# Performance work log

Hardware: AMD Instinct MI355X
Metric: run time of the kernel (lower is better)

Reference implementation:

```python
import jax, jax.numpy as jnp
import numpy as np

EMBED_DIM = 1024
HEAD_SIZE = 64
BATCH = 8
SEQ = 2048


def setup_inputs() -> dict:
    key = jax.random.key(0)
    k1, k2, k3, k4 = jax.random.split(key, 4)
    x = jax.random.normal(k1, (BATCH, SEQ, EMBED_DIM), dtype=jnp.float32)
    # Dense(use_bias=False) kernels: [in, out]
    scale = 1.0 / np.sqrt(EMBED_DIM)
    Wq = jax.random.normal(k2, (EMBED_DIM, HEAD_SIZE), dtype=jnp.float32) * scale
    Wk = jax.random.normal(k3, (EMBED_DIM, HEAD_SIZE), dtype=jnp.float32) * scale
    Wv = jax.random.normal(k4, (EMBED_DIM, HEAD_SIZE), dtype=jnp.float32) * scale
    return {"x": x, "Wq": Wq, "Wk": Wk, "Wv": Wv}


def reference(x, Wq, Wk, Wv):
    B, S, E = x.shape
    q = jnp.einsum("bse,eh->bsh", x, Wq)
    k = jnp.einsum("bse,eh->bsh", x, Wk)
    v = jnp.einsum("bse,eh->bsh", x, Wv)
    # scores scaled by embedding_dim**-0.5 (as in the original code)
    w = jnp.einsum("bqh,bkh->bqk", q, k) * (E ** -0.5)
    causal = jnp.tril(jnp.ones((S, S), dtype=bool))  # True on/below diag
    w = jnp.where(causal, w, -jnp.inf)
    w = jax.nn.softmax(w, axis=-1)
    # dropout is identity at inference
    return jnp.einsum("bqk,bkh->bqh", w, v)
```

## Files before the change

### kernel.cpp

```cpp
#include <hip/hip_runtime.h>
#include <hip/hip_bf16.h>


#define BATCH 8
#define SEQ   2048
#define EMB   1024
#define HD    64
#define ROWS  (BATCH*SEQ)
#define NTOT  192
#define BK    64
#define NKT   (EMB / BK)

typedef __attribute__((ext_vector_type(8))) short short8;
typedef __attribute__((ext_vector_type(4))) float floatx4;

static __device__ __forceinline__ short f2bf(float f) {
  union { __hip_bfloat16 h; short s; } u;
  u.h = __float2bfloat16(f);
  return u.s;
}

static __device__ __forceinline__ short8 pack8(float4 u, float4 v) {
  short8 r;
  r[0] = f2bf(u.x); r[1] = f2bf(u.y); r[2] = f2bf(u.z); r[3] = f2bf(u.w);
  r[4] = f2bf(v.x); r[5] = f2bf(v.y); r[6] = f2bf(v.z); r[7] = f2bf(v.w);
  return r;
}

static __device__ __forceinline__ void gload_lds16(const void* g, void* l) {
  __builtin_amdgcn_global_load_lds(
      (const __attribute__((address_space(1))) unsigned int*)g,
      (__attribute__((address_space(3))) unsigned int*)l, 16, 0, 0);
}

__global__ __launch_bounds__(256) void wt_kernel(
    const float* __restrict__ Wq, const float* __restrict__ Wk,
    const float* __restrict__ Wv, short* __restrict__ Wts) {
  const int id = blockIdx.x * 256 + threadIdx.x;
  const int kt = id / 1536;
  const int rem = id - kt * 1536;
  const int np = rem >> 3;
  const int s = rem & 7;
  const float* __restrict__ W = (np < 64) ? Wq : ((np < 128) ? Wk : Wv);
  const int n = np & 63;
  const int k0 = kt * BK + (s ^ (np & 7)) * 8;
  short8 o;
#pragma unroll
  for (int u = 0; u < 8; ++u) o[u] = f2bf(W[(size_t)(k0 + u) * HD + n]);
  *(short8*)(Wts + (size_t)id * 8) = o;
}

__global__ __launch_bounds__(256, 2) void proj_kernel(
    const float* __restrict__ x, const short* __restrict__ Wts,
    short* __restrict__ qb, short* __restrict__ kb_, short* __restrict__ vtb) {
  __shared__ __align__(16) float As[32 * 64];
  __shared__ __align__(16) short Bs[192 * 64];

  const int t = threadIdx.x, lane = t & 63, w = t >> 6;
  const int lo = lane & 15, quad = lane >> 4;
  const int e = lo & 7;
  const int m0 = blockIdx.x * 32;

  const int cc0 = w * 2, cc1 = cc0 + 1;
  const int ar0 = cc0 * 4 + (lane >> 4);
  const int ar1 = cc1 * 4 + (lane >> 4);
  const int aj = lane & 15;
  const float* agp0 = x + (size_t)(m0 + ar0) * EMB + ((aj ^ (ar0 & 7)) * 4);
  const float* agp1 = x + (size_t)(m0 + ar1) * EMB + ((aj ^ (ar1 & 7)) * 4);
  float* alp0 = As + cc0 * 256;
  float* alp1 = As + cc1 * 256;

  const short* bgp = Wts + (size_t)(w * 6) * 512 + lane * 8;
  short* blp = Bs + (w * 6) * 512;

  floatx4 acc[2][3];
#pragma unroll
  for (int mf = 0; mf < 2; ++mf)
#pragma unroll
    for (int j = 0; j < 3; ++j) acc[mf][j] = (floatx4){0.f, 0.f, 0.f, 0.f};

  for (int kt = 0; kt < NKT; ++kt) {
    __syncthreads();
    gload_lds16(agp0 + kt * BK, alp0);
    gload_lds16(agp1 + kt * BK, alp1);
    const short* bg = bgp + (size_t)kt * 12288;
#pragma unroll
    for (int i = 0; i < 6; ++i)
      gload_lds16(bg + i * 512, blp + i * 512);
    __syncthreads();

    short8 af[2][2];
#pragma unroll
    for (int mf = 0; mf < 2; ++mf) {
      const float* Ar = As + (mf * 16 + lo) * 64;
#pragma unroll
      for (int ks = 0; ks < 2; ++ks) {
        const float4 f0 = *(const float4*)(Ar + (((8 * ks + 2 * quad) ^ e) << 2));
        const float4 f1 = *(const float4*)(Ar + (((8 * ks + 2 * quad + 1) ^ e) << 2));
        af[mf][ks] = pack8(f0, f1);
      }
    }
    short8 bf[3][2];
#pragma unroll
    for (int j = 0; j < 3; ++j) {
      const short* Br = Bs + ((w * 3 + j) * 16 + lo) * 64;
#pragma unroll
      for (int ks = 0; ks < 2; ++ks)
        bf[j][ks] = *(const short8*)(Br + (((4 * ks + quad) ^ e) << 3));
    }
#pragma unroll
    for (int ks = 0; ks < 2; ++ks)
#pragma unroll
      for (int j = 0; j < 3; ++j) {
        acc[0][j] = __builtin_amdgcn_mfma_f32_16x16x32_bf16(af[0][ks], bf[j][ks], acc[0][j], 0, 0, 0);
        acc[1][j] = __builtin_amdgcn_mfma_f32_16x16x32_bf16(af[1][ks], bf[j][ks], acc[1][j], 0, 0, 0);
      }
  }

  const int bb = m0 >> 11;
  const int sbase = (m0 & (SEQ - 1)) + quad * 4;
#pragma unroll
  for (int mf = 0; mf < 2; ++mf) {
    const int rowb = m0 + mf * 16 + quad * 4;
#pragma unroll
    for (int j = 0; j < 3; ++j) {
      const int nt = w * 3 + j;
      const floatx4 v = acc[mf][j];
      if (nt < 4) {
#pragma unroll
        for (int r = 0; r < 4; ++r)
          qb[(size_t)(rowb + r) * HD + nt * 16 + lo] = f2bf(v[r] * 0.03125f);
      } else if (nt < 8) {
#pragma unroll
        for (int r = 0; r < 4; ++r)
          kb_[(size_t)(rowb + r) * HD + (nt - 4) * 16 + lo] = f2bf(v[r]);
      } else {
        const int col = (nt - 8) * 16 + lo;
        short4 sv = make_short4(f2bf(v[0]), f2bf(v[1]), f2bf(v[2]), f2bf(v[3]));
        *(short4*)(vtb + ((size_t)bb * HD + col) * SEQ + sbase + mf * 16) = sv;
      }
    }
  }
}

#define KSTR 72
#define PSTR 40

__global__ __launch_bounds__(256, 2) void attn_kernel(
    const short* __restrict__ qb, const short* __restrict__ kb,
    const short* __restrict__ vtb, float* __restrict__ out) {
  __shared__ __align__(16) short Ks[2][64 * KSTR];
  __shared__ __align__(16) short Vs[2][64 * KSTR];
  __shared__ __align__(16) short Ps[4][16 * PSTR];
  __shared__ __align__(16) floatx4 Red[2][5][64];

  const int b = blockIdx.y;
  const int bx = blockIdx.x;
  const int qx = (bx & 1) ? (63 - (bx >> 1)) : (bx >> 1);
  const int q0 = qx * 32;
  const int t = threadIdx.x, lane = t & 63, w = t >> 6;
  const int wr = w >> 1, wk = w & 1;
  const int lo = lane & 15, quad = lane >> 4;

  const short* qp = qb + ((size_t)b * SEQ + q0 + wr * 16 + lo) * HD + quad * 8;
  const short8 qf0 = *(const short8*)(qp);
  const short8 qf1 = *(const short8*)(qp + 32);

  const int r0 = t >> 3, c0 = (t & 7) * 8;
  const int r1 = r0 + 32;
  const short* __restrict__ kgb = kb + (size_t)b * SEQ * HD;
  const short* __restrict__ vgb = vtb + (size_t)b * HD * SEQ;

  floatx4 acc[4];
  float lsum[4] = {0.f, 0.f, 0.f, 0.f};
#pragma unroll
  for (int nt = 0; nt < 4; ++nt) acc[nt] = (floatx4){0.f, 0.f, 0.f, 0.f};

  {
    short8 k0v = *(const short8*)(kgb + (size_t)r0 * HD + c0);
    short8 k1v = *(const short8*)(kgb + (size_t)r1 * HD + c0);
    short8 v0v = *(const short8*)(vgb + (size_t)r0 * SEQ + c0);
    short8 v1v = *(const short8*)(vgb + (size_t)r1 * SEQ + c0);
    *(short8*)(&Ks[0][r0 * KSTR + c0]) = k0v;
    *(short8*)(&Ks[0][r1 * KSTR + c0]) = k1v;
    *(short8*)(&Vs[0][r0 * KSTR + c0]) = v0v;
    *(short8*)(&Vs[0][r1 * KSTR + c0]) = v1v;
  }

  const int niter = q0 / 64 + 1;
  for (int it = 0; it < niter; ++it) {
    const int j0 = it * 64;
    const int buf = it & 1;
    __syncthreads();

    short8 kfr[2][2], vfr[4];
#pragma unroll
    for (int n2 = 0; n2 < 2; ++n2) {
      const short* kr = &Ks[buf][(wk * 32 + n2 * 16 + lo) * KSTR + quad * 8];
      kfr[n2][0] = *(const short8*)(kr);
      kfr[n2][1] = *(const short8*)(kr + 32);
    }
#pragma unroll
    for (int nt = 0; nt < 4; ++nt)
      vfr[nt] = *(const short8*)(&Vs[buf][(nt * 16 + lo) * KSTR + wk * 32 + quad * 8]);

    short8 nk0, nk1, nv0, nv1;
    const bool more = (it + 1 < niter);
    if (more) {
      const int jn = j0 + 64;
      nk0 = *(const short8*)(kgb + (size_t)(jn + r0) * HD + c0);
      nk1 = *(const short8*)(kgb + (size_t)(jn + r1) * HD + c0);
      nv0 = *(const short8*)(vgb + (size_t)r0 * SEQ + jn + c0);
      nv1 = *(const short8*)(vgb + (size_t)r1 * SEQ + jn + c0);
    }

    floatx4 s0 = (floatx4){0.f, 0.f, 0.f, 0.f};
    floatx4 s1 = (floatx4){0.f, 0.f, 0.f, 0.f};
    s0 = __builtin_amdgcn_mfma_f32_16x16x32_bf16(qf0, kfr[0][0], s0, 0, 0, 0);
    s0 = __builtin_amdgcn_mfma_f32_16x16x32_bf16(qf1, kfr[0][1], s0, 0, 0, 0);
    s1 = __builtin_amdgcn_mfma_f32_16x16x32_bf16(qf0, kfr[1][0], s1, 0, 0, 0);
    s1 = __builtin_amdgcn_mfma_f32_16x16x32_bf16(qf1, kfr[1][1], s1, 0, 0, 0);

    const bool diag = (j0 + 64 > q0);
    const int rowb = q0 + wr * 16 + quad * 4;
    short* Pw = Ps[w];
#pragma unroll
    for (int r = 0; r < 4; ++r) {
      float e0 = __expf(s0[r]);
      float e1 = __expf(s1[r]);
      if (diag) {
        const int key0 = j0 + wk * 32 + lo;
        e0 = (key0 <= rowb + r) ? e0 : 0.f;
        e1 = (key0 + 16 <= rowb + r) ? e1 : 0.f;
      }
      lsum[r] += e0 + e1;
      Pw[(quad * 4 + r) * PSTR + lo] = f2bf(e0);
      Pw[(quad * 4 + r) * PSTR + 16 + lo] = f2bf(e1);
    }
    const short8 pf = *(const short8*)(&Pw[lo * PSTR + quad * 8]);
#pragma unroll
    for (int nt = 0; nt < 4; ++nt)
      acc[nt] = __builtin_amdgcn_mfma_f32_16x16x32_bf16(pf, vfr[nt], acc[nt], 0, 0, 0);

    if (more) {
      const int nb = buf ^ 1;
      *(short8*)(&Ks[nb][r0 * KSTR + c0]) = nk0;
      *(short8*)(&Ks[nb][r1 * KSTR + c0]) = nk1;
      *(short8*)(&Vs[nb][r0 * KSTR + c0]) = nv0;
      *(short8*)(&Vs[nb][r1 * KSTR + c0]) = nv1;
    }
  }

#pragma unroll
  for (int d = 1; d < 16; d <<= 1) {
#pragma unroll
    for (int r = 0; r < 4; ++r) lsum[r] += __shfl_xor(lsum[r], d);
  }

  if (wk == 1) {
#pragma unroll
    for (int nt = 0; nt < 4; ++nt) Red[wr][nt][lane] = acc[nt];
    Red[wr][4][lane] = (floatx4){lsum[0], lsum[1], lsum[2], lsum[3]};
  }
  __syncthreads();
  if (wk == 0) {
    const floatx4 lp = Red[wr][4][lane];
    const int rowb = q0 + wr * 16 + quad * 4;
#pragma unroll
    for (int nt = 0; nt < 4; ++nt) {
      const floatx4 o = acc[nt] + Red[wr][nt][lane];
#pragma unroll
      for (int r = 0; r < 4; ++r)
        out[((size_t)b * SEQ + rowb + r) * HD + nt * 16 + lo] =
            o[r] / (lsum[r] + lp[r]);
    }
  }
}

extern "C" void kernel_launch(void* const* d_in, const int* in_sizes, int n_in,
                              void* d_out, int out_size, void* d_ws, size_t ws_size,
                              hipStream_t stream) {
  const float* x  = (const float*)d_in[0];
  const float* Wq = (const float*)d_in[1];
  const float* Wk = (const float*)d_in[2];
  const float* Wv = (const float*)d_in[3];
  float* out = (float*)d_out;
  short* ws = (short*)d_ws;
  short* qbp = ws;
  short* kbp = ws + (size_t)ROWS * HD;
  short* vtp = ws + (size_t)2 * ROWS * HD;
  short* Wts = ws + (size_t)3 * ROWS * HD;

  wt_kernel<<<dim3(96), 256, 0, stream>>>(Wq, Wk, Wv, Wts);
  proj_kernel<<<dim3(ROWS / 32), 256, 0, stream>>>(x, Wts, qbp, kbp, vtp);
  attn_kernel<<<dim3(SEQ / 32, BATCH), 256, 0, stream>>>(qbp, kbp, vtp, out);
}
```

Measured before the change: 145.0 us.

## Shrink attention query tile to 16 rows and load K/V directly into swizzled LDS

The attention kernel now gives each block 16 query rows and two waves instead of 32 rows and four waves, which doubles the number of blocks. K and V tiles are copied with direct global-to-LDS loads into an XOR-swizzled layout with no padding, replacing register staging with a double buffer. The aim is to raise occupancy and cut register and VGPR traffic for tile loads. In exchange, every K/V tile is fetched by twice as many blocks, and the load is no longer prefetched, so each iteration adds a second barrier and exposes load latency.

```diff
diff --git a/kernel.cpp b/kernel.cpp
--- a/kernel.cpp
+++ b/kernel.cpp
@@ -143,75 +143,65 @@
   }
 }
 
-#define KSTR 72
+#define QT 16
 #define PSTR 40
 
-__global__ __launch_bounds__(256, 2) void attn_kernel(
+__global__ __launch_bounds__(128, 4) void attn_kernel(
     const short* __restrict__ qb, const short* __restrict__ kb,
     const short* __restrict__ vtb, float* __restrict__ out) {
-  __shared__ __align__(16) short Ks[2][64 * KSTR];
-  __shared__ __align__(16) short Vs[2][64 * KSTR];
-  __shared__ __align__(16) short Ps[4][16 * PSTR];
-  __shared__ __align__(16) floatx4 Red[2][5][64];
+  __shared__ __align__(16) short Ks[64 * 64];
+  __shared__ __align__(16) short Vs[64 * 64];
+  __shared__ __align__(16) short Ps[2][16 * PSTR];
+  __shared__ __align__(16) floatx4 Red[5][64];
 
   const int b = blockIdx.y;
   const int bx = blockIdx.x;
-  const int qx = (bx & 1) ? (63 - (bx >> 1)) : (bx >> 1);
-  const int q0 = qx * 32;
+  const int qx = (bx & 1) ? (127 - (bx >> 1)) : (bx >> 1);
+  const int q0 = qx * QT;
   const int t = threadIdx.x, lane = t & 63, w = t >> 6;
-  const int wr = w >> 1, wk = w & 1;
-  const int lo = lane & 15, quad = lane >> 4;
-
-  const short* qp = qb + ((size_t)b * SEQ + q0 + wr * 16 + lo) * HD + quad * 8;
+  const int lo = lane & 15, quad = lane >> 4, e = lo & 7;
+
+  const short* qp = qb + ((size_t)b * SEQ + q0 + lo) * HD + quad * 8;
   const short8 qf0 = *(const short8*)(qp);
   const short8 qf1 = *(const short8*)(qp + 32);
 
-  const int r0 = t >> 3, c0 = (t & 7) * 8;
-  const int r1 = r0 + 32;
-  const short* __restrict__ kgb = kb + (size_t)b * SEQ * HD;
-  const short* __restrict__ vgb = vtb + (size_t)b * HD * SEQ;
+  const int sr = lane >> 3;
+  const int jg = (lane & 7) ^ (sr & 7);
+  const short* kaddr = kb + (size_t)b * SEQ * HD + sr * HD + jg * 8;
+  const short* vaddr = vtb + (size_t)b * HD * SEQ + (size_t)sr * SEQ + jg * 8;
 
   floatx4 acc[4];
   float lsum[4] = {0.f, 0.f, 0.f, 0.f};
 #pragma unroll
   for (int nt = 0; nt < 4; ++nt) acc[nt] = (floatx4){0.f, 0.f, 0.f, 0.f};
-
-  {
-    short8 k0v = *(const short8*)(kgb + (size_t)r0 * HD + c0);
-    short8 k1v = *(const short8*)(kgb + (size_t)r1 * HD + c0);
-    short8 v0v = *(const short8*)(vgb + (size_t)r0 * SEQ + c0);
-    short8 v1v = *(const short8*)(vgb + (size_t)r1 * SEQ + c0);
-    *(short8*)(&Ks[0][r0 * KSTR + c0]) = k0v;
-    *(short8*)(&Ks[0][r1 * KSTR + c0]) = k1v;
-    *(short8*)(&Vs[0][r0 * KSTR + c0]) = v0v;
-    *(short8*)(&Vs[0][r1 * KSTR + c0]) = v1v;
-  }
 
   const int niter = q0 / 64 + 1;
   for (int it = 0; it < niter; ++it) {
     const int j0 = it * 64;
-    const int buf = it & 1;
-    __syncthreads();
-
-    short8 kfr[2][2], vfr[4];
+    __syncthreads();
+    if (w == 0) {
+#pragma unroll
+      for (int p = 0; p < 8; ++p)
+        gload_lds16(kaddr + (size_t)j0 * HD + p * 512, Ks + p * 512);
+    } else {
+#pragma unroll
+      for (int p = 0; p < 8; ++p)
+        gload_lds16(vaddr + (size_t)p * 8 * SEQ + j0, Vs + p * 512);
+    }
+    __syncthreads();
+
+    short8 kfr[2][2];
 #pragma unroll
     for (int n2 = 0; n2 < 2; ++n2) {
-      const short* kr = &Ks[buf][(wk * 32 + n2 * 16 + lo) * KSTR + quad * 8];
-      kfr[n2][0] = *(const short8*)(kr);
-      kfr[n2][1] = *(const short8*)(kr + 32);
-    }
-#pragma unroll
-    for (int nt = 0; nt < 4; ++nt)
-      vfr[nt] = *(const short8*)(&Vs[buf][(nt * 16 + lo) * KSTR + wk * 32 + quad * 8]);
-
-    short8 nk0, nk1, nv0, nv1;
-    const bool more = (it + 1 < niter);
-    if (more) {
-      const int jn = j0 + 64;
-      nk0 = *(const short8*)(kgb + (size_t)(jn + r0) * HD + c0);
-      nk1 = *(const short8*)(kgb + (size_t)(jn + r1) * HD + c0);
-      nv0 = *(const short8*)(vgb + (size_t)r0 * SEQ + jn + c0);
-      nv1 = *(const short8*)(vgb + (size_t)r1 * SEQ + jn + c0);
+      const int r = w * 32 + n2 * 16 + lo;
+      kfr[n2][0] = *(const short8*)(Ks + r * 64 + ((quad ^ e) << 3));
+      kfr[n2][1] = *(const short8*)(Ks + r * 64 + (((quad + 4) ^ e) << 3));
+    }
+    short8 vfr[4];
+#pragma unroll
+    for (int nt = 0; nt < 4; ++nt) {
+      const int d = nt * 16 + lo;
+      vfr[nt] = *(const short8*)(Vs + d * 64 + (((w * 4 + quad) ^ e) << 3));
     }
 
     floatx4 s0 = (floatx4){0.f, 0.f, 0.f, 0.f};
@@ -222,16 +212,16 @@
     s1 = __builtin_amdgcn_mfma_f32_16x16x32_bf16(qf1, kfr[1][1], s1, 0, 0, 0);
 
     const bool diag = (j0 + 64 > q0);
-    const int rowb = q0 + wr * 16 + quad * 4;
     short* Pw = Ps[w];
 #pragma unroll
     for (int r = 0; r < 4; ++r) {
       float e0 = __expf(s0[r]);
       float e1 = __expf(s1[r]);
       if (diag) {
-        const int key0 = j0 + wk * 32 + lo;
-        e0 = (key0 <= rowb + r) ? e0 : 0.f;
-        e1 = (key0 + 16 <= rowb + r) ? e1 : 0.f;
+        const int key0 = j0 + w * 32 + lo;
+        const int qrow = q0 + quad * 4 + r;
+        e0 = (key0 <= qrow) ? e0 : 0.f;
+        e1 = (key0 + 16 <= qrow) ? e1 : 0.f;
       }
       lsum[r] += e0 + e1;
       Pw[(quad * 4 + r) * PSTR + lo] = f2bf(e0);
@@ -241,14 +231,6 @@
 #pragma unroll
     for (int nt = 0; nt < 4; ++nt)
       acc[nt] = __builtin_amdgcn_mfma_f32_16x16x32_bf16(pf, vfr[nt], acc[nt], 0, 0, 0);
-
-    if (more) {
-      const int nb = buf ^ 1;
-      *(short8*)(&Ks[nb][r0 * KSTR + c0]) = nk0;
-      *(short8*)(&Ks[nb][r1 * KSTR + c0]) = nk1;
-      *(short8*)(&Vs[nb][r0 * KSTR + c0]) = nv0;
-      *(short8*)(&Vs[nb][r1 * KSTR + c0]) = nv1;
-    }
   }
 
 #pragma unroll
@@ -257,21 +239,20 @@
     for (int r = 0; r < 4; ++r) lsum[r] += __shfl_xor(lsum[r], d);
   }
 
-  if (wk == 1) {
-#pragma unroll
-    for (int nt = 0; nt < 4; ++nt) Red[wr][nt][lane] = acc[nt];
-    Red[wr][4][lane] = (floatx4){lsum[0], lsum[1], lsum[2], lsum[3]};
+  if (w == 1) {
+#pragma unroll
+    for (int nt = 0; nt < 4; ++nt) Red[nt][lane] = acc[nt];
+    Red[4][lane] = (floatx4){lsum[0], lsum[1], lsum[2], lsum[3]};
   }
   __syncthreads();
-  if (wk == 0) {
-    const floatx4 lp = Red[wr][4][lane];
-    const int rowb = q0 + wr * 16 + quad * 4;
+  if (w == 0) {
+    const floatx4 lp = Red[4][lane];
 #pragma unroll
     for (int nt = 0; nt < 4; ++nt) {
-      const floatx4 o = acc[nt] + Red[wr][nt][lane];
+      const floatx4 o = acc[nt] + Red[nt][lane];
 #pragma unroll
       for (int r = 0; r < 4; ++r)
-        out[((size_t)b * SEQ + rowb + r) * HD + nt * 16 + lo] =
+        out[((size_t)b * SEQ + q0 + quad * 4 + r) * HD + nt * 16 + lo] =
             o[r] / (lsum[r] + lp[r]);
     }
   }
@@ -293,5 +274,5 @@
 
   wt_kernel<<<dim3(96), 256, 0, stream>>>(Wq, Wk, Wv, Wts);
   proj_kernel<<<dim3(ROWS / 32), 256, 0, stream>>>(x, Wts, qbp, kbp, vtp);
-  attn_kernel<<<dim3(SEQ / 32, BATCH), 256, 0, stream>>>(qbp, kbp, vtp, out);
-}
+  attn_kernel<<<dim3(SEQ / QT, BATCH), 128, 0, stream>>>(qbp, kbp, vtp, out);
+}
```

New measurement: 146.6 us. No clear change (+1.2%).
